# Performance work log

Measured on AMD Instinct MI355X. Metric: run time of the kernel, lower is better.

Reference implementation:

```python
import jax, jax.numpy as jnp
import numpy as np

N, D, L, B = 100000, 1024, 128, 16
EPS = 1e-16  # torch_geometric softmax denominator eps


def setup_inputs() -> dict:
    key = jax.random.key(0)
    k_feat, k_b, k_wa, k_wb, k_wc = jax.random.split(key, 5)
    feature = jax.random.normal(k_feat, (N, D), dtype=jnp.float32)
    batch = jnp.sort(jax.random.randint(k_b, (N,), 0, B, dtype=jnp.int64))
    # xavier_normal_ init for the three Linear layers
    std_a = float(np.sqrt(2.0 / (D + L)))
    std_c = float(np.sqrt(2.0 / (L + 1)))
    Wa = jax.random.normal(k_wa, (L, D), dtype=jnp.float32) * std_a
    Wb = jax.random.normal(k_wb, (L, D), dtype=jnp.float32) * std_a
    Wc = jax.random.normal(k_wc, (1, L), dtype=jnp.float32) * std_c
    ba = jnp.zeros((L,), jnp.float32)
    bb = jnp.zeros((L,), jnp.float32)
    bc = jnp.zeros((1,), jnp.float32)
    return {"feature": feature, "batch": batch, "Wa": Wa, "ba": ba,
            "Wb": Wb, "bb": bb, "Wc": Wc, "bc": bc}


def reference(feature, batch, Wa, ba, Wb, bb, Wc, bc):
    # gated score MLP
    a = jax.nn.sigmoid(feature @ Wa.T + ba)          # [N, L]
    b = jnp.tanh(feature @ Wb.T + bb)                # [N, L]
    score = (a * b) @ Wc.T + bc                      # [N, 1]
    # segment softmax over bags (torch_geometric.utils.softmax)
    s = score[:, 0]                                  # [N]
    seg_max = jax.ops.segment_max(s, batch, num_segments=B)   # [B]
    e = jnp.exp(s - seg_max[batch])                  # [N]
    denom = jax.ops.segment_sum(e, batch, num_segments=B)     # [B]
    score_softmax = (e / (denom[batch] + EPS))[:, None]       # [N, 1]
    # scatter-sum weighted features per bag
    out = jax.ops.segment_sum(score_softmax * feature, batch, num_segments=B)  # [B, D]
    return (out, score, score_softmax, feature)
```

## Files before the change

kernel.cpp:

```cpp
#include <hip/hip_runtime.h>
#include <hip/hip_bf16.h>
#include <cmath>

#define NROWS 100000
#define DIM   1024
#define LH    128
#define NSEG  16
#define EPSF  1e-16f

#define OUT_OFF   0
#define SCORE_OFF (NSEG * DIM)
#define SM_OFF    (SCORE_OFF + NROWS)
#define FEAT_OFF  (SM_OFF + NROWS)

typedef __attribute__((ext_vector_type(4))) float floatx4;
typedef __attribute__((ext_vector_type(8))) short shortx8;

__device__ __forceinline__ unsigned short f2bf(float x) {
    unsigned u = __float_as_uint(x);
    u += 0x7FFFu + ((u >> 16) & 1u);
    return (unsigned short)(u >> 16);
}
__device__ __forceinline__ unsigned enc_f32(float f) {
    unsigned u = __float_as_uint(f);
    return (u & 0x80000000u) ? ~u : (u | 0x80000000u);
}
__device__ __forceinline__ float dec_f32(unsigned e) {
    unsigned u = (e & 0x80000000u) ? (e ^ 0x80000000u) : ~e;
    return __uint_as_float(u);
}

__global__ void init_kernel(const float* __restrict__ Wa,
                            const float* __restrict__ Wb,
                            unsigned short* __restrict__ wbf,
                            unsigned* __restrict__ segmax,
                            float* __restrict__ denom,
                            float* __restrict__ out) {
    int idx = blockIdx.x * 256 + threadIdx.x;
    if (idx < LH * DIM)
        wbf[idx] = f2bf(Wa[idx]);
    else if (idx < 2 * LH * DIM)
        wbf[idx] = f2bf(Wb[idx - LH * DIM]);
    if (idx < NSEG * DIM) out[OUT_OFF + idx] = 0.f;
    if (idx < NSEG) { segmax[idx] = 0u; denom[idx] = 0.f; }
}

__launch_bounds__(256)
__global__ void score_kernel(const float* __restrict__ feature,
                             const int* __restrict__ batch,
                             const unsigned short* __restrict__ wbf,
                             const float* __restrict__ ba,
                             const float* __restrict__ bb,
                             const float* __restrict__ wc,
                             const float* __restrict__ bc,
                             float* __restrict__ outp,
                             unsigned* __restrict__ segmax) {
    __shared__ __align__(16) unsigned short sA[64][72];
    __shared__ __align__(16) unsigned short sW[256][72];
    __shared__ float sBias[3 * LH];
    __shared__ float sScore[64];
    __shared__ int   sBatch[64];
    __shared__ unsigned sMax[NSEG];

    const int tid  = threadIdx.x;
    const int wave = tid >> 6;
    const int lane = tid & 63;
    const int q    = lane >> 4;
    const int c    = lane & 15;
    const int row0 = blockIdx.x * 64;

    if (tid < LH) {
        sBias[tid]          = ba[tid];
        sBias[LH + tid]     = bb[tid];
        sBias[2 * LH + tid] = wc[tid];
    }
    if (tid < NSEG) sMax[tid] = 0u;

    floatx4 acc[16];
#pragma unroll
    for (int t = 0; t < 16; ++t)
#pragma unroll
        for (int i = 0; i < 4; ++i) acc[t][i] = 0.f;

    for (int k0 = 0; k0 < DIM; k0 += 64) {
        __syncthreads();
        {
            const int rr = tid >> 4;
            const int cc = (tid & 15) << 2;
#pragma unroll
            for (int p = 0; p < 4; ++p) {
                const int r    = p * 16 + rr;
                const int grow = row0 + r;
                floatx4 v; v[0] = v[1] = v[2] = v[3] = 0.f;
                if (grow < NROWS) {
                    v = *(const floatx4*)(feature + (size_t)grow * DIM + k0 + cc);
                    *(floatx4*)(outp + FEAT_OFF + (size_t)grow * DIM + k0 + cc) = v;
                }
                sA[r][cc + 0] = f2bf(v[0]);
                sA[r][cc + 1] = f2bf(v[1]);
                sA[r][cc + 2] = f2bf(v[2]);
                sA[r][cc + 3] = f2bf(v[3]);
            }
        }
        {
#pragma unroll
            for (int p = 0; p < 8; ++p) {
                const int chunk = p * 256 + tid;
                const int r  = chunk >> 3;
                const int cc = (chunk & 7) << 3;
                shortx8 v = *(const shortx8*)(wbf + (size_t)r * DIM + k0 + cc);
                *(shortx8*)&sW[r][cc] = v;
            }
        }
        __syncthreads();
#pragma unroll
        for (int ks = 0; ks < 2; ++ks) {
            const int kk = ks * 32 + q * 8;
            shortx8 a = *(const shortx8*)&sA[wave * 16 + c][kk];
#pragma unroll
            for (int t = 0; t < 16; ++t) {
                shortx8 b = *(const shortx8*)&sW[t * 16 + c][kk];
                acc[t] = __builtin_amdgcn_mfma_f32_16x16x32_bf16(a, b, acc[t], 0, 0, 0);
            }
        }
    }

    float p4[4] = {0.f, 0.f, 0.f, 0.f};
#pragma unroll
    for (int t = 0; t < 8; ++t) {
        const int col = t * 16 + c;
        const float bav = sBias[col];
        const float bbv = sBias[LH + col];
        const float wcv = sBias[2 * LH + col];
#pragma unroll
        for (int i = 0; i < 4; ++i) {
            float u = acc[t][i] + bav;
            float v = acc[t + 8][i] + bbv;
            float sg = 1.f / (1.f + __expf(-u));
            float th = tanhf(v);
            p4[i] += sg * th * wcv;
        }
    }
#pragma unroll
    for (int i = 0; i < 4; ++i) {
        p4[i] += __shfl_xor(p4[i], 1, 16);
        p4[i] += __shfl_xor(p4[i], 2, 16);
        p4[i] += __shfl_xor(p4[i], 4, 16);
        p4[i] += __shfl_xor(p4[i], 8, 16);
    }

    __syncthreads();
    if (tid < 64) sBatch[tid] = -1;
    __syncthreads();

    const float bcv = bc[0];
    if (c == 0) {
#pragma unroll
        for (int i = 0; i < 4; ++i) {
            const int r    = wave * 16 + q * 4 + i;
            const int grow = row0 + r;
            if (grow < NROWS) {
                const float s = p4[i] + bcv;
                outp[SCORE_OFF + grow] = s;
                sScore[r] = s;
                sBatch[r] = batch[grow];
            }
        }
    }
    __syncthreads();
    if (tid < 64 && sBatch[tid] >= 0)
        atomicMax(&sMax[sBatch[tid]], enc_f32(sScore[tid]));
    __syncthreads();
    if (tid < NSEG && sMax[tid] != 0u)
        atomicMax(&segmax[tid], sMax[tid]);
}

__global__ void exp_kernel(const float* __restrict__ score,
                           const int* __restrict__ batch,
                           const unsigned* __restrict__ segmax,
                           float* __restrict__ evals,
                           float* __restrict__ denom) {
    __shared__ float sden[NSEG];
    const int tid = threadIdx.x;
    const int idx = blockIdx.x * 256 + tid;
    if (tid < NSEG) sden[tid] = 0.f;
    __syncthreads();
    if (idx < NROWS) {
        const int b = batch[idx];
        const float m = dec_f32(segmax[b]);
        const float e = expf(score[idx] - m);
        evals[idx] = e;
        atomicAdd(&sden[b], e);
    }
    __syncthreads();
    if (tid < NSEG && sden[tid] != 0.f) atomicAdd(&denom[tid], sden[tid]);
}

__launch_bounds__(256)
__global__ void wsum_kernel(const float* __restrict__ feature,
                            const int* __restrict__ batch,
                            const float* __restrict__ denom,
                            float* __restrict__ evals,
                            float* __restrict__ outp) {
    __shared__ float sw[128];
    __shared__ int   sb[128];
    const int tid = threadIdx.x;
    const int r0  = blockIdx.x * 128;

    if (tid < 128) {
        const int row = r0 + tid;
        if (row < NROWS) {
            const int b = batch[row];
            const float w = evals[row] / (denom[b] + EPSF);
            evals[row] = w;
            sw[tid] = w;
            sb[tid] = b;
        } else {
            sw[tid] = 0.f;
            sb[tid] = -1;
        }
    }
    __syncthreads();

    floatx4 acc; acc[0] = acc[1] = acc[2] = acc[3] = 0.f;
    int curseg = -1;
    const int cc = tid * 4;
    for (int r = 0; r < 128; ++r) {
        const int b = sb[r];
        if (b < 0) break;
        if (b != curseg) {
            if (curseg >= 0) {
#pragma unroll
                for (int j = 0; j < 4; ++j)
                    atomicAdd(&outp[OUT_OFF + curseg * DIM + cc + j], acc[j]);
            }
            curseg = b;
            acc[0] = acc[1] = acc[2] = acc[3] = 0.f;
        }
        const floatx4 f = *(const floatx4*)(feature + (size_t)(r0 + r) * DIM + cc);
        const float w = sw[r];
        acc[0] += w * f[0];
        acc[1] += w * f[1];
        acc[2] += w * f[2];
        acc[3] += w * f[3];
    }
    if (curseg >= 0) {
#pragma unroll
        for (int j = 0; j < 4; ++j)
            atomicAdd(&outp[OUT_OFF + curseg * DIM + cc + j], acc[j]);
    }
}

extern "C" void kernel_launch(void* const* d_in, const int* in_sizes, int n_in,
                              void* d_out, int out_size, void* d_ws, size_t ws_size,
                              hipStream_t stream) {
    const float* feature = (const float*)d_in[0];
    const int*   batch   = (const int*)d_in[1];
    const float* Wa      = (const float*)d_in[2];
    const float* ba      = (const float*)d_in[3];
    const float* Wb      = (const float*)d_in[4];
    const float* bb      = (const float*)d_in[5];
    const float* Wc      = (const float*)d_in[6];
    const float* bc      = (const float*)d_in[7];
    float* out = (float*)d_out;

    unsigned short* wbf = (unsigned short*)d_ws;
    unsigned* segmax = (unsigned*)((char*)d_ws + 2 * LH * DIM * 2);
    float*    denom  = (float*)((char*)d_ws + 2 * LH * DIM * 2 + 64);

    init_kernel<<<(2 * LH * DIM) / 256, 256, 0, stream>>>(Wa, Wb, wbf, segmax, denom, out);
    score_kernel<<<(NROWS + 63) / 64, 256, 0, stream>>>(feature, batch, wbf, ba, bb, Wc, bc, out, segmax);
    exp_kernel<<<(NROWS + 255) / 256, 256, 0, stream>>>(out + SCORE_OFF, batch, segmax, out + SM_OFF, denom);
    wsum_kernel<<<(NROWS + 127) / 128, 256, 0, stream>>>(feature, batch, denom, out + SM_OFF, out);
}
```

Baseline: 1.031 ms.

## Load GEMM operands directly from global, move feature copy to wsum, segment-indexed wsum

The score kernel no longer stages feature and weight tiles through shared memory. Each lane loads its fp32 feature slice straight from global memory, converts it to bf16 and feeds the MFMA, reading bf16 weights from global/L2 with no barriers. The feature passthrough copy moves from the score kernel into wsum. wsum now runs a per-segment 2D grid using segment starts found by binary search, and a separate norm kernel does the softmax normalisation. This drops shared-memory traffic and syncs, but makes weight reads uncached per wave and launches many empty wsum blocks (rows/128 × 16 segments).

```diff
diff --git a/kernel.cpp b/kernel.cpp
--- a/kernel.cpp
+++ b/kernel.cpp
@@ -7,6 +7,7 @@
 #define LH    128
 #define NSEG  16
 #define EPSF  1e-16f
+#define CHUNK 128
 
 #define OUT_OFF   0
 #define SCORE_OFF (NSEG * DIM)
@@ -32,9 +33,11 @@
 
 __global__ void init_kernel(const float* __restrict__ Wa,
                             const float* __restrict__ Wb,
+                            const int* __restrict__ batch,
                             unsigned short* __restrict__ wbf,
                             unsigned* __restrict__ segmax,
                             float* __restrict__ denom,
+                            int* __restrict__ segstart,
                             float* __restrict__ out) {
     int idx = blockIdx.x * 256 + threadIdx.x;
     if (idx < LH * DIM)
@@ -43,6 +46,15 @@
         wbf[idx] = f2bf(Wb[idx - LH * DIM]);
     if (idx < NSEG * DIM) out[OUT_OFF + idx] = 0.f;
     if (idx < NSEG) { segmax[idx] = 0u; denom[idx] = 0.f; }
+    if (blockIdx.x == 0 && threadIdx.x <= NSEG) {
+        const int b = threadIdx.x;
+        int lo = 0, hi = NROWS;
+        while (lo < hi) {
+            const int mid = (lo + hi) >> 1;
+            if (batch[mid] < b) lo = mid + 1; else hi = mid;
+        }
+        segstart[b] = lo;
+    }
 }
 
 __launch_bounds__(256)
@@ -55,8 +67,6 @@
                              const float* __restrict__ bc,
                              float* __restrict__ outp,
                              unsigned* __restrict__ segmax) {
-    __shared__ __align__(16) unsigned short sA[64][72];
-    __shared__ __align__(16) unsigned short sW[256][72];
     __shared__ float sBias[3 * LH];
     __shared__ float sScore[64];
     __shared__ int   sBatch[64];
@@ -75,6 +85,12 @@
         sBias[2 * LH + tid] = wc[tid];
     }
     if (tid < NSEG) sMax[tid] = 0u;
+    if (tid < 64)   sBatch[tid] = -1;
+
+    const int rowA  = row0 + wave * 16 + c;
+    const int rowAs = rowA < NROWS ? rowA : (NROWS - 1);
+    const float* __restrict__ arow = feature + (size_t)rowAs * DIM + q * 8;
+    const unsigned short* __restrict__ wbase = wbf + (size_t)c * DIM + q * 8;
 
     floatx4 acc[16];
 #pragma unroll
@@ -82,46 +98,19 @@
 #pragma unroll
         for (int i = 0; i < 4; ++i) acc[t][i] = 0.f;
 
-    for (int k0 = 0; k0 < DIM; k0 += 64) {
-        __syncthreads();
-        {
-            const int rr = tid >> 4;
-            const int cc = (tid & 15) << 2;
-#pragma unroll
-            for (int p = 0; p < 4; ++p) {
-                const int r    = p * 16 + rr;
-                const int grow = row0 + r;
-                floatx4 v; v[0] = v[1] = v[2] = v[3] = 0.f;
-                if (grow < NROWS) {
-                    v = *(const floatx4*)(feature + (size_t)grow * DIM + k0 + cc);
-                    *(floatx4*)(outp + FEAT_OFF + (size_t)grow * DIM + k0 + cc) = v;
-                }
-                sA[r][cc + 0] = f2bf(v[0]);
-                sA[r][cc + 1] = f2bf(v[1]);
-                sA[r][cc + 2] = f2bf(v[2]);
-                sA[r][cc + 3] = f2bf(v[3]);
-            }
-        }
-        {
-#pragma unroll
-            for (int p = 0; p < 8; ++p) {
-                const int chunk = p * 256 + tid;
-                const int r  = chunk >> 3;
-                const int cc = (chunk & 7) << 3;
-                shortx8 v = *(const shortx8*)(wbf + (size_t)r * DIM + k0 + cc);
-                *(shortx8*)&sW[r][cc] = v;
-            }
-        }
-        __syncthreads();
-#pragma unroll
-        for (int ks = 0; ks < 2; ++ks) {
-            const int kk = ks * 32 + q * 8;
-            shortx8 a = *(const shortx8*)&sA[wave * 16 + c][kk];
-#pragma unroll
-            for (int t = 0; t < 16; ++t) {
-                shortx8 b = *(const shortx8*)&sW[t * 16 + c][kk];
-                acc[t] = __builtin_amdgcn_mfma_f32_16x16x32_bf16(a, b, acc[t], 0, 0, 0);
-            }
+#pragma unroll 2
+    for (int k0 = 0; k0 < DIM; k0 += 32) {
+        const floatx4 a0 = *(const floatx4*)(arow + k0);
+        const floatx4 a1 = *(const floatx4*)(arow + k0 + 4);
+        shortx8 af;
+        af[0] = (short)f2bf(a0[0]); af[1] = (short)f2bf(a0[1]);
+        af[2] = (short)f2bf(a0[2]); af[3] = (short)f2bf(a0[3]);
+        af[4] = (short)f2bf(a1[0]); af[5] = (short)f2bf(a1[1]);
+        af[6] = (short)f2bf(a1[2]); af[7] = (short)f2bf(a1[3]);
+#pragma unroll
+        for (int t = 0; t < 16; ++t) {
+            const shortx8 bf = *(const shortx8*)(wbase + (size_t)t * 16 * DIM + k0);
+            acc[t] = __builtin_amdgcn_mfma_f32_16x16x32_bf16(af, bf, acc[t], 0, 0, 0);
         }
     }
 
@@ -149,8 +138,6 @@
         p4[i] += __shfl_xor(p4[i], 8, 16);
     }
 
-    __syncthreads();
-    if (tid < 64) sBatch[tid] = -1;
     __syncthreads();
 
     const float bcv = bc[0];
@@ -196,59 +183,47 @@
     if (tid < NSEG && sden[tid] != 0.f) atomicAdd(&denom[tid], sden[tid]);
 }
 
+__global__ void norm_kernel(const int* __restrict__ batch,
+                            const float* __restrict__ denom,
+                            float* __restrict__ evals) {
+    const int idx = blockIdx.x * 256 + threadIdx.x;
+    if (idx < NROWS)
+        evals[idx] = evals[idx] / (denom[batch[idx]] + EPSF);
+}
+
 __launch_bounds__(256)
 __global__ void wsum_kernel(const float* __restrict__ feature,
-                            const int* __restrict__ batch,
-                            const float* __restrict__ denom,
-                            float* __restrict__ evals,
+                            const int* __restrict__ segstart,
+                            const float* __restrict__ sm,
                             float* __restrict__ outp) {
-    __shared__ float sw[128];
-    __shared__ int   sb[128];
+    const int s   = blockIdx.y;
+    const int beg = segstart[s];
+    const int end = segstart[s + 1];
+    const int r0  = beg + blockIdx.x * CHUNK;
+    if (r0 >= end) return;
+    const int nr = min(CHUNK, end - r0);
+
+    __shared__ float sw[CHUNK];
     const int tid = threadIdx.x;
-    const int r0  = blockIdx.x * 128;
-
-    if (tid < 128) {
-        const int row = r0 + tid;
-        if (row < NROWS) {
-            const int b = batch[row];
-            const float w = evals[row] / (denom[b] + EPSF);
-            evals[row] = w;
-            sw[tid] = w;
-            sb[tid] = b;
-        } else {
-            sw[tid] = 0.f;
-            sb[tid] = -1;
-        }
-    }
-    __syncthreads();
-
+    if (tid < CHUNK) sw[tid] = (tid < nr) ? sm[r0 + tid] : 0.f;
+    __syncthreads();
+
+    const int cc = tid * 4;
     floatx4 acc; acc[0] = acc[1] = acc[2] = acc[3] = 0.f;
-    int curseg = -1;
-    const int cc = tid * 4;
-    for (int r = 0; r < 128; ++r) {
-        const int b = sb[r];
-        if (b < 0) break;
-        if (b != curseg) {
-            if (curseg >= 0) {
-#pragma unroll
-                for (int j = 0; j < 4; ++j)
-                    atomicAdd(&outp[OUT_OFF + curseg * DIM + cc + j], acc[j]);
-            }
-            curseg = b;
-            acc[0] = acc[1] = acc[2] = acc[3] = 0.f;
-        }
-        const floatx4 f = *(const floatx4*)(feature + (size_t)(r0 + r) * DIM + cc);
+#pragma unroll 4
+    for (int r = 0; r < nr; ++r) {
+        const float* __restrict__ src = feature + (size_t)(r0 + r) * DIM + cc;
+        const floatx4 f = *(const floatx4*)src;
+        *(floatx4*)(outp + FEAT_OFF + (size_t)(r0 + r) * DIM + cc) = f;
         const float w = sw[r];
         acc[0] += w * f[0];
         acc[1] += w * f[1];
         acc[2] += w * f[2];
         acc[3] += w * f[3];
     }
-    if (curseg >= 0) {
-#pragma unroll
-        for (int j = 0; j < 4; ++j)
-            atomicAdd(&outp[OUT_OFF + curseg * DIM + cc + j], acc[j]);
-    }
+#pragma unroll
+    for (int j = 0; j < 4; ++j)
+        atomicAdd(&outp[OUT_OFF + s * DIM + cc + j], acc[j]);
 }
 
 extern "C" void kernel_launch(void* const* d_in, const int* in_sizes, int n_in,
@@ -264,12 +239,20 @@
     const float* bc      = (const float*)d_in[7];
     float* out = (float*)d_out;
 
-    unsigned short* wbf = (unsigned short*)d_ws;
-    unsigned* segmax = (unsigned*)((char*)d_ws + 2 * LH * DIM * 2);
-    float*    denom  = (float*)((char*)d_ws + 2 * LH * DIM * 2 + 64);
-
-    init_kernel<<<(2 * LH * DIM) / 256, 256, 0, stream>>>(Wa, Wb, wbf, segmax, denom, out);
-    score_kernel<<<(NROWS + 63) / 64, 256, 0, stream>>>(feature, batch, wbf, ba, bb, Wc, bc, out, segmax);
-    exp_kernel<<<(NROWS + 255) / 256, 256, 0, stream>>>(out + SCORE_OFF, batch, segmax, out + SM_OFF, denom);
-    wsum_kernel<<<(NROWS + 127) / 128, 256, 0, stream>>>(feature, batch, denom, out + SM_OFF, out);
-}
+    char* ws = (char*)d_ws;
+    unsigned short* wbf    = (unsigned short*)ws;
+    unsigned*       segmax = (unsigned*)(ws + 2 * LH * DIM * 2);
+    float*          denom  = (float*)(ws + 2 * LH * DIM * 2 + 64);
+    int*            segst  = (int*)(ws + 2 * LH * DIM * 2 + 128);
+
+    init_kernel<<<(2 * LH * DIM) / 256, 256, 0, stream>>>(
+        Wa, Wb, batch, wbf, segmax, denom, segst, out);
+    score_kernel<<<(NROWS + 63) / 64, 256, 0, stream>>>(
+        feature, batch, wbf, ba, bb, Wc, bc, out, segmax);
+    exp_kernel<<<(NROWS + 255) / 256, 256, 0, stream>>>(
+        out + SCORE_OFF, batch, segmax, out + SM_OFF, denom);
+    norm_kernel<<<(NROWS + 255) / 256, 256, 0, stream>>>(
+        batch, denom, out + SM_OFF);
+    dim3 wgrid((NROWS + CHUNK - 1) / CHUNK, NSEG);
+    wsum_kernel<<<wgrid, 256, 0, stream>>>(feature, segst, out + SM_OFF, out);
+}
```

New measurement: 1.226 ms. +18.9%, slower.
